# Kernel optimization log

Hardware: AMD Instinct MI355X
Metric: run time of the kernel (lower is better)

Reference implementation:

```python
import jax, jax.numpy as jnp
import numpy as np

DIM = 256
HEADS = 8
HEAD_DIM = DIM // HEADS
EDGE_TYPES = 8  # edge_type_count; table has EDGE_TYPES+1 rows, row 0 is padding
B, N = 2, 2048
EPS = 1e-5


def layer_norm(x, g, b):
    mu = jnp.mean(x, axis=-1, keepdims=True)
    var = jnp.mean(jnp.square(x - mu), axis=-1, keepdims=True)
    return (x - mu) * jax.lax.rsqrt(var + EPS) * g + b


def setup_inputs() -> dict:
    key = jax.random.key(0)
    ks = jax.random.split(key, 12)
    s = 0.02
    x = jax.random.normal(ks[0], (B, N, DIM), dtype=jnp.float32)
    edge_types = jax.random.randint(ks[1], (B, N, N), 0, EDGE_TYPES + 1, dtype=jnp.int32)
    node_mask = jax.random.randint(ks[2], (B, N), 0, 2, dtype=jnp.int32).astype(bool)
    qkv_w = jax.random.normal(ks[3], (DIM, 3 * DIM), dtype=jnp.float32) * s
    qkv_b = jnp.zeros((3 * DIM,), jnp.float32)
    proj_w = jax.random.normal(ks[4], (DIM, DIM), dtype=jnp.float32) * s
    proj_b = jnp.zeros((DIM,), jnp.float32)
    edge_bias_table = jax.random.normal(ks[5], (EDGE_TYPES + 1, HEADS), dtype=jnp.float32) * s
    edge_bias_table = edge_bias_table.at[0].set(0.0)  # padding_idx=0
    ln1_g = jnp.ones((DIM,), jnp.float32); ln1_b = jnp.zeros((DIM,), jnp.float32)
    ln2_g = jnp.ones((DIM,), jnp.float32); ln2_b = jnp.zeros((DIM,), jnp.float32)
    ffn_w1 = jax.random.normal(ks[6], (DIM, 4 * DIM), dtype=jnp.float32) * s
    ffn_b1 = jnp.zeros((4 * DIM,), jnp.float32)
    ffn_w2 = jax.random.normal(ks[7], (4 * DIM, DIM), dtype=jnp.float32) * s
    ffn_b2 = jnp.zeros((DIM,), jnp.float32)
    return dict(x=x, edge_types=edge_types, node_mask=node_mask,
                qkv_w=qkv_w, qkv_b=qkv_b, proj_w=proj_w, proj_b=proj_b,
                edge_bias_table=edge_bias_table, ln1_g=ln1_g, ln1_b=ln1_b,
                ln2_g=ln2_g, ln2_b=ln2_b, ffn_w1=ffn_w1, ffn_b1=ffn_b1,
                ffn_w2=ffn_w2, ffn_b2=ffn_b2)


def reference(x, edge_types, node_mask, qkv_w, qkv_b, proj_w, proj_b,
              edge_bias_table, ln1_g, ln1_b, ln2_g, ln2_b,
              ffn_w1, ffn_b1, ffn_w2, ffn_b2):
    scale = HEAD_DIM ** -0.5
    residual = x
    h = layer_norm(x, ln1_g, ln1_b)
    qkv = h @ qkv_w + qkv_b                         # [B,N,3*DIM]
    qkv = qkv.reshape(B, N, 3, HEADS, HEAD_DIM)
    q, k, v = (qkv[:, :, 0].transpose(0, 2, 1, 3),  # [B,H,N,d]
               qkv[:, :, 1].transpose(0, 2, 1, 3),
               qkv[:, :, 2].transpose(0, 2, 1, 3))
    scores = jnp.einsum('bhnd,bhmd->bhnm', q, k) * scale
    bias = edge_bias_table[edge_types]              # [B,N,N,H]
    scores = scores + bias.transpose(0, 3, 1, 2)    # [B,H,N,N]
    eye = jnp.eye(N, dtype=bool)
    edge_mask = (edge_types != 0) | eye[None]
    node_mask_2d = node_mask[:, None, :] & node_mask[:, :, None]
    attn_mask = edge_mask & node_mask_2d            # [B,N,N]
    scores = jnp.where(attn_mask[:, None], scores, -1e9)
    attn = jax.nn.softmax(scores, axis=-1)
    out = jnp.einsum('bhnm,bhmd->bhnd', attn, v)
    out = out.transpose(0, 2, 1, 3).reshape(B, N, DIM)
    out = (out @ proj_w + proj_b) * node_mask[:, :, None]
    x1 = residual + out
    h2 = layer_norm(x1, ln2_g, ln2_b)
    h2 = jax.nn.gelu(h2 @ ffn_w1 + ffn_b1, approximate=False) @ ffn_w2 + ffn_b2
    h2 = h2 * node_mask[:, :, None]
    return x1 + h2
```

## Files before the change

### kernel.cpp

```cpp
#include <hip/hip_runtime.h>
#include <math.h>

#define DIMM 256
#define HEADS 8
#define NB 2048
#define BB 2
#define ROWS (BB*NB)

typedef __attribute__((ext_vector_type(8))) short bf16x8;
typedef __attribute__((ext_vector_type(4))) short bf16x4;
typedef __attribute__((ext_vector_type(4))) float f32x4;

__device__ inline unsigned short f2bf(float f) {
    unsigned int u = __float_as_uint(f);
    u += 0x7FFFu + ((u >> 16) & 1u);
    return (unsigned short)(u >> 16);
}
__device__ inline float bf2f(unsigned short u) {
    return __uint_as_float(((unsigned int)u) << 16);
}

__device__ inline int get_mask(const void* nm, int fmt, int idx) {
    if (fmt) return ((const unsigned char*)nm)[idx] != 0;
    return ((const int*)nm)[idx] != 0;
}

__device__ inline void ln8_body(const float* __restrict__ x, const float* __restrict__ g,
                                const float* __restrict__ bb, unsigned short* __restrict__ o,
                                int row, int lane32) {
    int c0 = lane32 * 8;
    float4 v0 = *(const float4*)&x[(size_t)row * DIMM + c0];
    float4 v1 = *(const float4*)&x[(size_t)row * DIMM + c0 + 4];
    float s  = v0.x + v0.y + v0.z + v0.w + v1.x + v1.y + v1.z + v1.w;
    float s2 = v0.x*v0.x + v0.y*v0.y + v0.z*v0.z + v0.w*v0.w
             + v1.x*v1.x + v1.y*v1.y + v1.z*v1.z + v1.w*v1.w;
#pragma unroll
    for (int off = 16; off >= 1; off >>= 1) {
        s  += __shfl_xor(s,  off);
        s2 += __shfl_xor(s2, off);
    }
    float mean = s * (1.0f / DIMM);
    float var  = s2 * (1.0f / DIMM) - mean * mean;
    float rstd = rsqrtf(var + 1e-5f);
    float4 g0 = *(const float4*)&g[c0],  g1 = *(const float4*)&g[c0 + 4];
    float4 b0 = *(const float4*)&bb[c0], b1 = *(const float4*)&bb[c0 + 4];
    ushort4 u0, u1;
    u0.x = f2bf((v0.x - mean) * rstd * g0.x + b0.x);
    u0.y = f2bf((v0.y - mean) * rstd * g0.y + b0.y);
    u0.z = f2bf((v0.z - mean) * rstd * g0.z + b0.z);
    u0.w = f2bf((v0.w - mean) * rstd * g0.w + b0.w);
    u1.x = f2bf((v1.x - mean) * rstd * g1.x + b1.x);
    u1.y = f2bf((v1.y - mean) * rstd * g1.y + b1.y);
    u1.z = f2bf((v1.z - mean) * rstd * g1.z + b1.z);
    u1.w = f2bf((v1.w - mean) * rstd * g1.w + b1.w);
    *(ushort4*)&o[(size_t)row * DIMM + c0]     = u0;
    *(ushort4*)&o[(size_t)row * DIMM + c0 + 4] = u1;
}

__global__ __launch_bounds__(256) void prep_kernel(
    const float* __restrict__ w0, const float* __restrict__ w1,
    const float* __restrict__ w2, const float* __restrict__ w3,
    unsigned short* __restrict__ o0, unsigned short* __restrict__ o1,
    unsigned short* __restrict__ o2, unsigned short* __restrict__ o3,
    const float* __restrict__ x, const float* __restrict__ ln1_g,
    const float* __restrict__ ln1_b, unsigned short* __restrict__ h_ln,
    const int* __restrict__ etypes, const void* __restrict__ nmask,
    unsigned char* __restrict__ emaskP)
{
    __shared__ float tile[64][65];
    __shared__ int fsh;
    int bid = blockIdx.x, t = threadIdx.x;
    if (bid < 192) {
        const float* src; unsigned short* dst; int K, N, idx;
        if (bid < 48)       { src = w0; dst = o0; K = 256;  N = 768;  idx = bid; }
        else if (bid < 64)  { src = w1; dst = o1; K = 256;  N = 256;  idx = bid - 48; }
        else if (bid < 128) { src = w2; dst = o2; K = 256;  N = 1024; idx = bid - 64; }
        else                { src = w3; dst = o3; K = 1024; N = 256;  idx = bid - 128; }
        int ntiles = N >> 6;
        int k0 = (idx / ntiles) * 64, n0 = (idx % ntiles) * 64;
        int r = t >> 4, c4 = (t & 15) * 4;
#pragma unroll
        for (int i = 0; i < 4; ++i) {
            float4 v = *(const float4*)&src[(size_t)(k0 + r + i * 16) * N + n0 + c4];
            tile[r + i * 16][c4 + 0] = v.x;
            tile[r + i * 16][c4 + 1] = v.y;
            tile[r + i * 16][c4 + 2] = v.z;
            tile[r + i * 16][c4 + 3] = v.w;
        }
        __syncthreads();
#pragma unroll
        for (int i = 0; i < 4; ++i) {
            int n = n0 + r + i * 16;
            ushort4 u;
            u.x = f2bf(tile[c4 + 0][r + i * 16]);
            u.y = f2bf(tile[c4 + 1][r + i * 16]);
            u.z = f2bf(tile[c4 + 2][r + i * 16]);
            u.w = f2bf(tile[c4 + 3][r + i * 16]);
            *(ushort4*)&dst[(size_t)n * K + k0 + c4] = u;
        }
    } else if (bid < 704) {
        int row = (bid - 192) * 8 + (t >> 5);
        ln8_body(x, ln1_g, ln1_b, h_ln, row, t & 31);
    } else {
        if (t == 0) fsh = 0;
        __syncthreads();
        if (((const unsigned char*)nmask)[4 * t + 1] != 0) fsh = 1;
        __syncthreads();
        int fm = fsh;
        int unit = (bid - 704) * 4 + (t >> 6);
        int lane = t & 63, quad = lane >> 4, l15 = lane & 15;
        int b = unit >> 12;
        int qt16 = (unit >> 5) & 127;
        int kt = unit & 31;
        int qr = qt16 * 16 + l15;
        int rowv = get_mask(nmask, fm, b * NB + qr);
        const int* erow = etypes + (size_t)(b * NB + qr) * NB;
        int dw[4];
#pragma unroll
        for (int t16 = 0; t16 < 4; ++t16) {
            int col0 = kt * 64 + t16 * 16 + quad * 4;
            int4 e4 = *(const int4*)(erow + col0);
            int ee[4] = {e4.x, e4.y, e4.z, e4.w};
            int cv[4];
            if (fm) {
                unsigned int m4 = *(const unsigned int*)((const unsigned char*)nmask + b * NB + col0);
                cv[0] = (m4 & 0xffu) != 0;     cv[1] = (m4 & 0xff00u) != 0;
                cv[2] = (m4 & 0xff0000u) != 0; cv[3] = (m4 >> 24) != 0;
            } else {
                int4 m4 = *(const int4*)((const int*)nmask + b * NB + col0);
                cv[0] = m4.x != 0; cv[1] = m4.y != 0; cv[2] = m4.z != 0; cv[3] = m4.w != 0;
            }
            unsigned int pk = 0u;
#pragma unroll
            for (int r = 0; r < 4; ++r) {
                int col = col0 + r;
                int valid = rowv && cv[r] && ((ee[r] != 0) || (col == qr));
                pk |= (valid ? (unsigned int)(ee[r] + 1) : 0u) << (r * 8);
            }
            dw[t16] = (int)pk;
        }
        int4 o = {dw[0], dw[1], dw[2], dw[3]};
        *(int4*)(emaskP + (size_t)unit * 1024 + lane * 16) = o;
    }
}

__global__ __launch_bounds__(256) void gemm_qkv_mfma(
    const unsigned short* __restrict__ A, const unsigned short* __restrict__ Bt,
    const float* __restrict__ bias,
    unsigned short* __restrict__ qkvh, unsigned short* __restrict__ vT)
{
    const int K = 256;
    int t = threadIdx.x, w = t >> 6, l = t & 63;
    int l15 = l & 15, quad = l >> 4;
    int n0 = blockIdx.x * 64;
    int m0 = blockIdx.y * 64;
    const unsigned short* ap = A + (size_t)(m0 + w * 16 + l15) * K + quad * 8;
    const unsigned short* bp = Bt + (size_t)(n0 + l15) * K + quad * 8;

    f32x4 acc[4];
#pragma unroll
    for (int c = 0; c < 4; ++c) acc[c] = (f32x4){0.f, 0.f, 0.f, 0.f};

    bf16x8 aA, bA[4], aB, bB[4];
    auto ld = [&](bf16x8& af, bf16x8 (&bf)[4], int k0) {
        af = *(const bf16x8*)(ap + k0);
#pragma unroll
        for (int c = 0; c < 4; ++c)
            bf[c] = *(const bf16x8*)(bp + (size_t)(c * 16) * K + k0);
    };
    auto pr = [&](const bf16x8& af, const bf16x8 (&bf)[4]) {
#pragma unroll
        for (int c = 0; c < 4; ++c)
            acc[c] = __builtin_amdgcn_mfma_f32_16x16x32_bf16(af, bf[c], acc[c], 0, 0, 0);
    };
    ld(aA, bA, 0);
    for (int k0 = 0; k0 < K; k0 += 64) {
        ld(aB, bB, k0 + 32);
        pr(aA, bA);
        if (k0 + 64 < K) ld(aA, bA, k0 + 64);
        pr(aB, bB);
    }

    if (n0 < 512) {
        float sc = (n0 < 256) ? 0.17677669529663689f : 1.0f;
#pragma unroll
        for (int r = 0; r < 4; ++r) {
            int row = m0 + w * 16 + quad * 4 + r;
#pragma unroll
            for (int c = 0; c < 4; ++c) {
                int col = n0 + c * 16 + l15;
                qkvh[(size_t)row * 512 + col] = f2bf((acc[c][r] + bias[col]) * sc);
            }
        }
    } else {
        int bb_ = m0 >> 11;
        int n = (m0 + w * 16 + quad * 4) & 2047;
#pragma unroll
        for (int c = 0; c < 4; ++c) {
            int col = n0 + c * 16 + l15 - 512;
            int hidx = col >> 5, d = col & 31;
            float bs = bias[n0 + c * 16 + l15];
            ushort4 u;
            u.x = f2bf(acc[c][0] + bs);
            u.y = f2bf(acc[c][1] + bs);
            u.z = f2bf(acc[c][2] + bs);
            u.w = f2bf(acc[c][3] + bs);
            *(ushort4*)&vT[(size_t)((bb_ * HEADS + hidx) * 32 + d) * NB + n] = u;
        }
    }
}

__global__ __launch_bounds__(256) void attn_mfma(
    const unsigned short* __restrict__ qkvh,
    const unsigned short* __restrict__ vT,
    const unsigned char* __restrict__ emaskP,
    const float* __restrict__ table,
    unsigned short* __restrict__ OpH, float* __restrict__ lpart)
{
    __shared__ unsigned short P[4][16][72];
    __shared__ float tab2m[16];

    int t = threadIdx.x;
    int w = t >> 6, l = t & 63;
    int l15 = l & 15, quad = l >> 4;
    int h = blockIdx.x;
    int qt = blockIdx.y;
    int z = blockIdx.z, b = z >> 2, sp = z & 3;
    int q0 = qt * 64 + w * 16;
    int kbase = sp * (NB / 4);

    if (t < 16) tab2m[t] = (t >= 1 && t < 10) ? __expf(table[(t - 1) * 8 + h]) : 0.f;
    __syncthreads();

    bf16x8 bq = *(const bf16x8*)(qkvh + (size_t)(b * NB + q0 + l15) * 512 + h * 32 + quad * 8);

    const unsigned short* kp = qkvh + (size_t)(b * NB + l15) * 512 + 256 + h * 32 + quad * 8;
    const unsigned short* vp = vT + (size_t)((b * HEADS + h) * 32 + l15) * NB + quad * 8;
    int qt16 = qt * 4 + w;
    const unsigned char* ep = emaskP + (size_t)((b * 128 + qt16) * 32) * 1024 + l * 16;

    float lacc = 0.f;
    f32x4 O0 = {0.f, 0.f, 0.f, 0.f}, O1 = {0.f, 0.f, 0.f, 0.f};

    bf16x8 kA[4], kB[4];
    bf16x8 vA[2][2], vB[2][2];
    int4 eA, eB;

    auto loadtile = [&](bf16x8 (&kf)[4], bf16x8 (&vf)[2][2], int4& ef, int m0) {
#pragma unroll
        for (int t16 = 0; t16 < 4; ++t16)
            kf[t16] = *(const bf16x8*)(kp + (size_t)(m0 + t16 * 16) * 512);
#pragma unroll
        for (int ks = 0; ks < 2; ++ks) {
            vf[ks][0] = *(const bf16x8*)(vp + m0 + ks * 32);
            vf[ks][1] = *(const bf16x8*)(vp + 16 * NB + m0 + ks * 32);
        }
        ef = *(const int4*)(ep + (size_t)(m0 >> 6) * 1024);
    };

    auto process = [&](const bf16x8 (&kf)[4], const bf16x8 (&vf)[2][2], const int4& ef) {
        int ew[4] = {ef.x, ef.y, ef.z, ef.w};
#pragma unroll
        for (int t16 = 0; t16 < 4; ++t16) {
            f32x4 zero = {0.f, 0.f, 0.f, 0.f};
            f32x4 sT = __builtin_amdgcn_mfma_f32_16x16x32_bf16(kf[t16], bq, zero, 0, 0, 0);
            unsigned int e = (unsigned int)ew[t16];
            float p0 = __expf(sT[0]) * tab2m[e & 0xffu];
            float p1 = __expf(sT[1]) * tab2m[(e >> 8) & 0xffu];
            float p2 = __expf(sT[2]) * tab2m[(e >> 16) & 0xffu];
            float p3 = __expf(sT[3]) * tab2m[e >> 24];
            lacc += (p0 + p1) + (p2 + p3);
            bf16x4 pb;
            pb[0] = (short)f2bf(p0); pb[1] = (short)f2bf(p1);
            pb[2] = (short)f2bf(p2); pb[3] = (short)f2bf(p3);
            *(bf16x4*)&P[w][l15][t16 * 16 + quad * 4] = pb;
        }
#pragma unroll
        for (int ks = 0; ks < 2; ++ks) {
            bf16x8 pa = *(const bf16x8*)&P[w][l15][ks * 32 + quad * 8];
            O0 = __builtin_amdgcn_mfma_f32_16x16x32_bf16(pa, vf[ks][0], O0, 0, 0, 0);
            O1 = __builtin_amdgcn_mfma_f32_16x16x32_bf16(pa, vf[ks][1], O1, 0, 0, 0);
        }
    };

    loadtile(kA, vA, eA, kbase);
    for (int m0 = kbase; m0 < kbase + NB / 4; m0 += 128) {
        loadtile(kB, vB, eB, m0 + 64);
        process(kA, vA, eA);
        if (m0 + 128 < kbase + NB / 4) loadtile(kA, vA, eA, m0 + 128);
        process(kB, vB, eB);
    }

    lacc += __shfl_xor(lacc, 16);
    lacc += __shfl_xor(lacc, 32);

    unsigned short* Ob = OpH + (size_t)sp * ROWS * DIMM;
#pragma unroll
    for (int r = 0; r < 4; ++r) {
        int row = b * NB + q0 + quad * 4 + r;
        Ob[(size_t)row * DIMM + h * 32 + l15]      = f2bf(O0[r]);
        Ob[(size_t)row * DIMM + h * 32 + 16 + l15] = f2bf(O1[r]);
    }
    if (quad == 0) {
        int row = b * NB + q0 + l15;
        lpart[(size_t)sp * ROWS * 8 + (size_t)row * 8 + h] = lacc;
    }
}

__global__ __launch_bounds__(1024) void megaback(
    const unsigned short* __restrict__ OpH, const float* __restrict__ lpart,
    const unsigned short* __restrict__ projT, const float* __restrict__ proj_b,
    const float* __restrict__ x, const void* __restrict__ nmask,
    const float* __restrict__ g2, const float* __restrict__ b2,
    const unsigned short* __restrict__ f1T, const float* __restrict__ ffn_b1,
    const unsigned short* __restrict__ f2T, const float* __restrict__ ffn_b2,
    float* __restrict__ out)
{
    __shared__ float rinv_l[16][8];
    __shared__ float stats[16][2];
    __shared__ float redn[16][16][2];
    __shared__ unsigned short Astage[16][264];
    __shared__ float x1s[16][260];
    __shared__ unsigned short hstage[16][264];
    __shared__ unsigned short midstage[16][1032];
    __shared__ int fsh;

    int t = threadIdx.x;
    int w = t >> 6, l = t & 63;
    int l15 = l & 15, quad = l >> 4;
    int grow0 = blockIdx.x * 16;

    if (t == 0) fsh = 0;
    __syncthreads();
    if (((const unsigned char*)nmask)[4 * t + 1] != 0) fsh = 1;

    if (t < 128) {
        int row = t >> 3, h = t & 7;
        float s = 0.f;
#pragma unroll
        for (int sp = 0; sp < 4; ++sp)
            s += lpart[(size_t)sp * ROWS * 8 + (size_t)(grow0 + row) * 8 + h];
        rinv_l[row][h] = (s > 0.f) ? 1.f / s : 0.f;
    }
    __syncthreads();
    int fm = fsh;

    {
        int row = t >> 6, col4 = (t & 63) * 4;
        float rinv = rinv_l[row][col4 >> 5];
        float o0 = 0.f, o1 = 0.f, o2 = 0.f, o3 = 0.f;
#pragma unroll
        for (int sp = 0; sp < 4; ++sp) {
            ushort4 u = *(const ushort4*)&OpH[(size_t)sp * ROWS * DIMM +
                                             (size_t)(grow0 + row) * DIMM + col4];
            o0 += bf2f(u.x); o1 += bf2f(u.y); o2 += bf2f(u.z); o3 += bf2f(u.w);
        }
        ushort4 u;
        u.x = f2bf(o0 * rinv); u.y = f2bf(o1 * rinv);
        u.z = f2bf(o2 * rinv); u.w = f2bf(o3 * rinv);
        *(ushort4*)&Astage[row][col4] = u;
    }
    __syncthreads();

    {
        int col = w * 16 + l15;
        f32x4 acc = (f32x4){0.f, 0.f, 0.f, 0.f};
        const unsigned short* bp = projT + (size_t)col * 256 + quad * 8;
        bf16x8 sb[4];
#pragma unroll
        for (int i = 0; i < 4; ++i) sb[i] = *(const bf16x8*)(bp + i * 32);
#pragma unroll
        for (int ch = 0; ch < 8; ++ch) {
            bf16x8 a = *(const bf16x8*)&Astage[l15][ch * 32 + quad * 8];
            acc = __builtin_amdgcn_mfma_f32_16x16x32_bf16(a, sb[ch & 3], acc, 0, 0, 0);
            if (ch + 4 < 8) sb[ch & 3] = *(const bf16x8*)(bp + (ch + 4) * 32);
        }
        float bs = proj_b[col];
#pragma unroll
        for (int r = 0; r < 4; ++r) {
            int row = quad * 4 + r, grow = grow0 + row;
            float mk = (float)get_mask(nmask, fm, grow);
            float v = (acc[r] + bs) * mk + x[(size_t)grow * DIMM + col];
            x1s[row][col] = v;
            float s = v, s2 = v * v;
#pragma unroll
            for (int off = 1; off < 16; off <<= 1) {
                s += __shfl_xor(s, off); s2 += __shfl_xor(s2, off);
            }
            if (l15 == 0) { redn[row][w][0] = s; redn[row][w][1] = s2; }
        }
    }
    __syncthreads();
    if (t < 16) {
        float s = 0.f, s2 = 0.f;
#pragma unroll
        for (int ww = 0; ww < 16; ++ww) { s += redn[t][ww][0]; s2 += redn[t][ww][1]; }
        float mean = s * (1.f / DIMM);
        float var  = s2 * (1.f / DIMM) - mean * mean;
        stats[t][0] = mean; stats[t][1] = rsqrtf(var + 1e-5f);
    }
    __syncthreads();

    {
        int col = w * 16 + l15;
        float gv = g2[col], bv = b2[col];
#pragma unroll
        for (int r = 0; r < 4; ++r) {
            int row = quad * 4 + r;
            float hv = (x1s[row][col] - stats[row][0]) * stats[row][1] * gv + bv;
            hstage[row][col] = f2bf(hv);
        }
    }
    __syncthreads();

    {
        f32x4 acc[4];
#pragma unroll
        for (int c = 0; c < 4; ++c) acc[c] = (f32x4){0.f, 0.f, 0.f, 0.f};
        const unsigned short* bp = f1T + (size_t)(w * 64 + l15) * 256 + quad * 8;
        bf16x8 bA[4], bB[4];
#pragma unroll
        for (int c = 0; c < 4; ++c) bA[c] = *(const bf16x8*)(bp + (size_t)(c * 16) * 256);
#pragma unroll
        for (int ch = 0; ch < 8; ++ch) {
            bf16x8 a = *(const bf16x8*)&hstage[l15][ch * 32 + quad * 8];
            if (ch + 1 < 8) {
#pragma unroll
                for (int c = 0; c < 4; ++c)
                    bB[c] = *(const bf16x8*)(bp + (size_t)(c * 16) * 256 + (ch + 1) * 32);
            }
#pragma unroll
            for (int c = 0; c < 4; ++c)
                acc[c] = __builtin_amdgcn_mfma_f32_16x16x32_bf16(a, bA[c], acc[c], 0, 0, 0);
#pragma unroll
            for (int c = 0; c < 4; ++c) bA[c] = bB[c];
        }
#pragma unroll
        for (int c = 0; c < 4; ++c) {
            int col = w * 64 + c * 16 + l15;
            float bs = ffn_b1[col];
#pragma unroll
            for (int r = 0; r < 4; ++r) {
                float v = acc[c][r] + bs;
                float x2 = v * v;
                float p = v * fmaf(0.07135481f, x2, 1.5957691f);
                float e = __expf(p);
                float gl = v * (e / (e + 1.f));
                midstage[quad * 4 + r][col] = f2bf(gl);
            }
        }
    }
    __syncthreads();

    {
        int col = w * 16 + l15;
        f32x4 acc = (f32x4){0.f, 0.f, 0.f, 0.f};
        const unsigned short* bp = f2T + (size_t)col * 1024 + quad * 8;
        bf16x8 sb[4];
#pragma unroll
        for (int i = 0; i < 4; ++i) sb[i] = *(const bf16x8*)(bp + i * 32);
#pragma unroll
        for (int ch = 0; ch < 32; ++ch) {
            bf16x8 a = *(const bf16x8*)&midstage[l15][ch * 32 + quad * 8];
            acc = __builtin_amdgcn_mfma_f32_16x16x32_bf16(a, sb[ch & 3], acc, 0, 0, 0);
            if (ch + 4 < 32) sb[ch & 3] = *(const bf16x8*)(bp + (ch + 4) * 32);
        }
        float bs = ffn_b2[col];
#pragma unroll
        for (int r = 0; r < 4; ++r) {
            int row = quad * 4 + r, grow = grow0 + row;
            float mk = (float)get_mask(nmask, fm, grow);
            out[(size_t)grow * DIMM + col] = x1s[row][col] + (acc[r] + bs) * mk;
        }
    }
}

extern "C" void kernel_launch(void* const* d_in, const int* in_sizes, int n_in,
                              void* d_out, int out_size, void* d_ws, size_t ws_size,
                              hipStream_t stream) {
    const float* x       = (const float*)d_in[0];
    const int*   etypes  = (const int*)d_in[1];
    const void*  nmask   = d_in[2];
    const float* qkv_w   = (const float*)d_in[3];
    const float* qkv_b   = (const float*)d_in[4];
    const float* proj_w  = (const float*)d_in[5];
    const float* proj_b  = (const float*)d_in[6];
    const float* table   = (const float*)d_in[7];
    const float* ln1_g   = (const float*)d_in[8];
    const float* ln1_b   = (const float*)d_in[9];
    const float* ln2_g   = (const float*)d_in[10];
    const float* ln2_b   = (const float*)d_in[11];
    const float* ffn_w1  = (const float*)d_in[12];
    const float* ffn_b1  = (const float*)d_in[13];
    const float* ffn_w2  = (const float*)d_in[14];
    const float* ffn_b2  = (const float*)d_in[15];
    float* out = (float*)d_out;
    float* ws  = (float*)d_ws;

    float* lpart = ws;
    unsigned short* ub = (unsigned short*)(ws + 131072);
    unsigned short* h_ln   = ub;
    unsigned short* qkvh   = ub + 1048576;
    unsigned short* vT     = ub + 3145728;
    unsigned short* OpH    = ub + 4194304;
    unsigned short* qkvT   = ub + 8388608;
    unsigned short* projT  = ub + 8585216;
    unsigned short* f1T    = ub + 8650752;
    unsigned short* f2T    = ub + 8912896;
    unsigned char* emaskP  = (unsigned char*)(ub + 9175040);

    prep_kernel<<<dim3(2752), dim3(256), 0, stream>>>(
        qkv_w, proj_w, ffn_w1, ffn_w2, qkvT, projT, f1T, f2T,
        x, ln1_g, ln1_b, h_ln, etypes, nmask, emaskP);
    gemm_qkv_mfma<<<dim3(12, 64), dim3(256), 0, stream>>>(h_ln, qkvT, qkv_b, qkvh, vT);
    attn_mfma<<<dim3(HEADS, NB/64, BB*4), dim3(256), 0, stream>>>(
        qkvh, vT, emaskP, table, OpH, lpart);
    megaback<<<dim3(ROWS/16), dim3(1024), 0, stream>>>(
        OpH, lpart, projT, proj_b, x, nmask, ln2_g, ln2_b,
        f1T, ffn_b1, f2T, ffn_b2, out);
}
```

Before: 230.1 us.

## Pack edge mask to 4-bit codes, halve megaback row tile, add occupancy hints

The precomputed edge-type/mask buffer now packs each entry into 4 bits instead of 8, which halves the mask traffic read by the attention kernel. megaback processes 8 rows per block instead of 16, doubling the grid. The MFMA inputs still use 16 rows, so half of each tile's compute is duplicated and masked off. Register double-buffering in the FFN GEMMs is removed and launch_bounds occupancy hints are added, trading latency hiding for lower register pressure and more resident waves.

```diff
diff --git a/kernel.cpp b/kernel.cpp
--- a/kernel.cpp
+++ b/kernel.cpp
@@ -115,7 +115,7 @@
         int qr = qt16 * 16 + l15;
         int rowv = get_mask(nmask, fm, b * NB + qr);
         const int* erow = etypes + (size_t)(b * NB + qr) * NB;
-        int dw[4];
+        unsigned int dw[2] = {0u, 0u};
 #pragma unroll
         for (int t16 = 0; t16 < 4; ++t16) {
             int col0 = kt * 64 + t16 * 16 + quad * 4;
@@ -130,17 +130,16 @@
                 int4 m4 = *(const int4*)((const int*)nmask + b * NB + col0);
                 cv[0] = m4.x != 0; cv[1] = m4.y != 0; cv[2] = m4.z != 0; cv[3] = m4.w != 0;
             }
-            unsigned int pk = 0u;
 #pragma unroll
             for (int r = 0; r < 4; ++r) {
                 int col = col0 + r;
                 int valid = rowv && cv[r] && ((ee[r] != 0) || (col == qr));
-                pk |= (valid ? (unsigned int)(ee[r] + 1) : 0u) << (r * 8);
-            }
-            dw[t16] = (int)pk;
-        }
-        int4 o = {dw[0], dw[1], dw[2], dw[3]};
-        *(int4*)(emaskP + (size_t)unit * 1024 + lane * 16) = o;
+                unsigned int code = valid ? (unsigned int)(ee[r] + 1) : 0u;
+                dw[t16 >> 1] |= code << ((t16 & 1) * 16 + r * 4);
+            }
+        }
+        int2 o = {(int)dw[0], (int)dw[1]};
+        *(int2*)(emaskP + (size_t)unit * 512 + lane * 8) = o;
     }
 }
 
@@ -210,7 +209,7 @@
     }
 }
 
-__global__ __launch_bounds__(256) void attn_mfma(
+__global__ __launch_bounds__(256, 8) void attn_mfma(
     const unsigned short* __restrict__ qkvh,
     const unsigned short* __restrict__ vT,
     const unsigned char* __restrict__ emaskP,
@@ -237,16 +236,16 @@
     const unsigned short* kp = qkvh + (size_t)(b * NB + l15) * 512 + 256 + h * 32 + quad * 8;
     const unsigned short* vp = vT + (size_t)((b * HEADS + h) * 32 + l15) * NB + quad * 8;
     int qt16 = qt * 4 + w;
-    const unsigned char* ep = emaskP + (size_t)((b * 128 + qt16) * 32) * 1024 + l * 16;
+    const unsigned char* ep = emaskP + (size_t)((b * 128 + qt16) * 32) * 512 + l * 8;
 
     float lacc = 0.f;
     f32x4 O0 = {0.f, 0.f, 0.f, 0.f}, O1 = {0.f, 0.f, 0.f, 0.f};
 
     bf16x8 kA[4], kB[4];
     bf16x8 vA[2][2], vB[2][2];
-    int4 eA, eB;
-
-    auto loadtile = [&](bf16x8 (&kf)[4], bf16x8 (&vf)[2][2], int4& ef, int m0) {
+    int2 eA, eB;
+
+    auto loadtile = [&](bf16x8 (&kf)[4], bf16x8 (&vf)[2][2], int2& ef, int m0) {
 #pragma unroll
         for (int t16 = 0; t16 < 4; ++t16)
             kf[t16] = *(const bf16x8*)(kp + (size_t)(m0 + t16 * 16) * 512);
@@ -255,20 +254,19 @@
             vf[ks][0] = *(const bf16x8*)(vp + m0 + ks * 32);
             vf[ks][1] = *(const bf16x8*)(vp + 16 * NB + m0 + ks * 32);
         }
-        ef = *(const int4*)(ep + (size_t)(m0 >> 6) * 1024);
+        ef = *(const int2*)(ep + (size_t)(m0 >> 6) * 512);
     };
 
-    auto process = [&](const bf16x8 (&kf)[4], const bf16x8 (&vf)[2][2], const int4& ef) {
-        int ew[4] = {ef.x, ef.y, ef.z, ef.w};
+    auto process = [&](const bf16x8 (&kf)[4], const bf16x8 (&vf)[2][2], const int2& ef) {
 #pragma unroll
         for (int t16 = 0; t16 < 4; ++t16) {
             f32x4 zero = {0.f, 0.f, 0.f, 0.f};
             f32x4 sT = __builtin_amdgcn_mfma_f32_16x16x32_bf16(kf[t16], bq, zero, 0, 0, 0);
-            unsigned int e = (unsigned int)ew[t16];
-            float p0 = __expf(sT[0]) * tab2m[e & 0xffu];
-            float p1 = __expf(sT[1]) * tab2m[(e >> 8) & 0xffu];
-            float p2 = __expf(sT[2]) * tab2m[(e >> 16) & 0xffu];
-            float p3 = __expf(sT[3]) * tab2m[e >> 24];
+            unsigned int e = ((unsigned int)((t16 < 2) ? ef.x : ef.y)) >> ((t16 & 1) * 16);
+            float p0 = __expf(sT[0]) * tab2m[e & 0xFu];
+            float p1 = __expf(sT[1]) * tab2m[(e >> 4) & 0xFu];
+            float p2 = __expf(sT[2]) * tab2m[(e >> 8) & 0xFu];
+            float p3 = __expf(sT[3]) * tab2m[(e >> 12) & 0xFu];
             lacc += (p0 + p1) + (p2 + p3);
             bf16x4 pb;
             pb[0] = (short)f2bf(p0); pb[1] = (short)f2bf(p1);
@@ -307,7 +305,7 @@
     }
 }
 
-__global__ __launch_bounds__(1024) void megaback(
+__global__ __launch_bounds__(1024, 8) void megaback(
     const unsigned short* __restrict__ OpH, const float* __restrict__ lpart,
     const unsigned short* __restrict__ projT, const float* __restrict__ proj_b,
     const float* __restrict__ x, const void* __restrict__ nmask,
@@ -316,25 +314,25 @@
     const unsigned short* __restrict__ f2T, const float* __restrict__ ffn_b2,
     float* __restrict__ out)
 {
-    __shared__ float rinv_l[16][8];
-    __shared__ float stats[16][2];
-    __shared__ float redn[16][16][2];
-    __shared__ unsigned short Astage[16][264];
-    __shared__ float x1s[16][260];
-    __shared__ unsigned short hstage[16][264];
-    __shared__ unsigned short midstage[16][1032];
+    __shared__ float rinv_l[8][8];
+    __shared__ float stats[8][2];
+    __shared__ float redn[8][16][2];
+    __shared__ unsigned short Astage[8][264];
+    __shared__ float x1s[8][260];
+    __shared__ unsigned short hstage[8][264];
+    __shared__ unsigned short midstage[8][1032];
     __shared__ int fsh;
 
     int t = threadIdx.x;
     int w = t >> 6, l = t & 63;
     int l15 = l & 15, quad = l >> 4;
-    int grow0 = blockIdx.x * 16;
+    int grow0 = blockIdx.x * 8;
 
     if (t == 0) fsh = 0;
     __syncthreads();
     if (((const unsigned char*)nmask)[4 * t + 1] != 0) fsh = 1;
 
-    if (t < 128) {
+    if (t < 64) {
         int row = t >> 3, h = t & 7;
         float s = 0.f;
 #pragma unroll
@@ -345,7 +343,7 @@
     __syncthreads();
     int fm = fsh;
 
-    {
+    if (t < 512) {
         int row = t >> 6, col4 = (t & 63) * 4;
         float rinv = rinv_l[row][col4 >> 5];
         float o0 = 0.f, o1 = 0.f, o2 = 0.f, o3 = 0.f;
@@ -371,27 +369,30 @@
         for (int i = 0; i < 4; ++i) sb[i] = *(const bf16x8*)(bp + i * 32);
 #pragma unroll
         for (int ch = 0; ch < 8; ++ch) {
-            bf16x8 a = *(const bf16x8*)&Astage[l15][ch * 32 + quad * 8];
+            bf16x8 a = *(const bf16x8*)&Astage[l15 & 7][ch * 32 + quad * 8];
             acc = __builtin_amdgcn_mfma_f32_16x16x32_bf16(a, sb[ch & 3], acc, 0, 0, 0);
             if (ch + 4 < 8) sb[ch & 3] = *(const bf16x8*)(bp + (ch + 4) * 32);
         }
         float bs = proj_b[col];
 #pragma unroll
         for (int r = 0; r < 4; ++r) {
-            int row = quad * 4 + r, grow = grow0 + row;
-            float mk = (float)get_mask(nmask, fm, grow);
-            float v = (acc[r] + bs) * mk + x[(size_t)grow * DIMM + col];
-            x1s[row][col] = v;
-            float s = v, s2 = v * v;
-#pragma unroll
-            for (int off = 1; off < 16; off <<= 1) {
-                s += __shfl_xor(s, off); s2 += __shfl_xor(s2, off);
-            }
-            if (l15 == 0) { redn[row][w][0] = s; redn[row][w][1] = s2; }
-        }
-    }
-    __syncthreads();
-    if (t < 16) {
+            int row16 = quad * 4 + r;
+            if (row16 < 8) {
+                int grow = grow0 + row16;
+                float mk = (float)get_mask(nmask, fm, grow);
+                float v = (acc[r] + bs) * mk + x[(size_t)grow * DIMM + col];
+                x1s[row16][col] = v;
+                float s = v, s2 = v * v;
+#pragma unroll
+                for (int off = 1; off < 16; off <<= 1) {
+                    s += __shfl_xor(s, off); s2 += __shfl_xor(s2, off);
+                }
+                if (l15 == 0) { redn[row16][w][0] = s; redn[row16][w][1] = s2; }
+            }
+        }
+    }
+    __syncthreads();
+    if (t < 8) {
         float s = 0.f, s2 = 0.f;
 #pragma unroll
         for (int ww = 0; ww < 16; ++ww) { s += redn[t][ww][0]; s2 += redn[t][ww][1]; }
@@ -406,9 +407,11 @@
         float gv = g2[col], bv = b2[col];
 #pragma unroll
         for (int r = 0; r < 4; ++r) {
-            int row = quad * 4 + r;
-            float hv = (x1s[row][col] - stats[row][0]) * stats[row][1] * gv + bv;
-            hstage[row][col] = f2bf(hv);
+            int row16 = quad * 4 + r;
+            if (row16 < 8) {
+                float hv = (x1s[row16][col] - stats[row16][0]) * stats[row16][1] * gv + bv;
+                hstage[row16][col] = f2bf(hv);
+            }
         }
     }
     __syncthreads();
@@ -418,22 +421,14 @@
 #pragma unroll
         for (int c = 0; c < 4; ++c) acc[c] = (f32x4){0.f, 0.f, 0.f, 0.f};
         const unsigned short* bp = f1T + (size_t)(w * 64 + l15) * 256 + quad * 8;
-        bf16x8 bA[4], bB[4];
-#pragma unroll
-        for (int c = 0; c < 4; ++c) bA[c] = *(const bf16x8*)(bp + (size_t)(c * 16) * 256);
 #pragma unroll
         for (int ch = 0; ch < 8; ++ch) {
-            bf16x8 a = *(const bf16x8*)&hstage[l15][ch * 32 + quad * 8];
-            if (ch + 1 < 8) {
-#pragma unroll
-                for (int c = 0; c < 4; ++c)
-                    bB[c] = *(const bf16x8*)(bp + (size_t)(c * 16) * 256 + (ch + 1) * 32);
-            }
-#pragma unroll
-            for (int c = 0; c < 4; ++c)
-                acc[c] = __builtin_amdgcn_mfma_f32_16x16x32_bf16(a, bA[c], acc[c], 0, 0, 0);
-#pragma unroll
-            for (int c = 0; c < 4; ++c) bA[c] = bB[c];
+            bf16x8 a = *(const bf16x8*)&hstage[l15 & 7][ch * 32 + quad * 8];
+#pragma unroll
+            for (int c = 0; c < 4; ++c) {
+                bf16x8 bw = *(const bf16x8*)(bp + (size_t)(c * 16) * 256 + ch * 32);
+                acc[c] = __builtin_amdgcn_mfma_f32_16x16x32_bf16(a, bw, acc[c], 0, 0, 0);
+            }
         }
 #pragma unroll
         for (int c = 0; c < 4; ++c) {
@@ -441,12 +436,15 @@
             float bs = ffn_b1[col];
 #pragma unroll
             for (int r = 0; r < 4; ++r) {
-                float v = acc[c][r] + bs;
-                float x2 = v * v;
-                float p = v * fmaf(0.07135481f, x2, 1.5957691f);
-                float e = __expf(p);
-                float gl = v * (e / (e + 1.f));
-                midstage[quad * 4 + r][col] = f2bf(gl);
+                int row16 = quad * 4 + r;
+                if (row16 < 8) {
+                    float v = acc[c][r] + bs;
+                    float x2 = v * v;
+                    float p = v * fmaf(0.07135481f, x2, 1.5957691f);
+                    float e = __expf(p);
+                    float gl = v * (e / (e + 1.f));
+                    midstage[row16][col] = f2bf(gl);
+                }
             }
         }
     }
@@ -454,23 +452,28 @@
 
     {
         int col = w * 16 + l15;
-        f32x4 acc = (f32x4){0.f, 0.f, 0.f, 0.f};
+        f32x4 acc0 = (f32x4){0.f, 0.f, 0.f, 0.f};
+        f32x4 acc1 = (f32x4){0.f, 0.f, 0.f, 0.f};
         const unsigned short* bp = f2T + (size_t)col * 1024 + quad * 8;
-        bf16x8 sb[4];
-#pragma unroll
-        for (int i = 0; i < 4; ++i) sb[i] = *(const bf16x8*)(bp + i * 32);
-#pragma unroll
-        for (int ch = 0; ch < 32; ++ch) {
-            bf16x8 a = *(const bf16x8*)&midstage[l15][ch * 32 + quad * 8];
-            acc = __builtin_amdgcn_mfma_f32_16x16x32_bf16(a, sb[ch & 3], acc, 0, 0, 0);
-            if (ch + 4 < 32) sb[ch & 3] = *(const bf16x8*)(bp + (ch + 4) * 32);
-        }
+#pragma unroll
+        for (int ch = 0; ch < 16; ++ch) {
+            bf16x8 a0 = *(const bf16x8*)&midstage[l15 & 7][ch * 32 + quad * 8];
+            bf16x8 w0 = *(const bf16x8*)(bp + ch * 32);
+            acc0 = __builtin_amdgcn_mfma_f32_16x16x32_bf16(a0, w0, acc0, 0, 0, 0);
+            bf16x8 a1 = *(const bf16x8*)&midstage[l15 & 7][(ch + 16) * 32 + quad * 8];
+            bf16x8 w1 = *(const bf16x8*)(bp + (ch + 16) * 32);
+            acc1 = __builtin_amdgcn_mfma_f32_16x16x32_bf16(a1, w1, acc1, 0, 0, 0);
+        }
+        f32x4 acc = acc0 + acc1;
         float bs = ffn_b2[col];
 #pragma unroll
         for (int r = 0; r < 4; ++r) {
-            int row = quad * 4 + r, grow = grow0 + row;
-            float mk = (float)get_mask(nmask, fm, grow);
-            out[(size_t)grow * DIMM + col] = x1s[row][col] + (acc[r] + bs) * mk;
+            int row16 = quad * 4 + r;
+            if (row16 < 8) {
+                int grow = grow0 + row16;
+                float mk = (float)get_mask(nmask, fm, grow);
+                out[(size_t)grow * DIMM + col] = x1s[row16][col] + (acc[r] + bs) * mk;
+            }
         }
     }
 }
@@ -515,7 +518,7 @@
     gemm_qkv_mfma<<<dim3(12, 64), dim3(256), 0, stream>>>(h_ln, qkvT, qkv_b, qkvh, vT);
     attn_mfma<<<dim3(HEADS, NB/64, BB*4), dim3(256), 0, stream>>>(
         qkvh, vT, emaskP, table, OpH, lpart);
-    megaback<<<dim3(ROWS/16), dim3(1024), 0, stream>>>(
+    megaback<<<dim3(ROWS/8), dim3(1024), 0, stream>>>(
         OpH, lpart, projT, proj_b, x, nmask, ln2_g, ln2_b,
         f1T, ffn_b1, f2T, ffn_b2, out);
 }
```

Result: slower. 364.7 us (+58.5%).

## Compact valid query rows and pack edge codes to 4 bits in attention

Applied to the files above, without the earlier changes.

Adds a scan kernel that counts masked-in nodes per batch, builds a compacted list of valid query row indices, and zeroes lpart for masked-out rows. The edge-mask prep and the attention kernel then iterate only over compacted query tiles and exit early past the valid count. This skips roughly half the query work when about half the nodes are masked. Edge codes are also packed as 4-bit nibbles instead of bytes, halving emaskP traffic. The cost is an extra small serial launch and gather indirection, and rows left unwritten must be handled correctly downstream.

```diff
diff --git a/kernel.cpp b/kernel.cpp
--- a/kernel.cpp
+++ b/kernel.cpp
@@ -23,6 +23,57 @@
 __device__ inline int get_mask(const void* nm, int fmt, int idx) {
     if (fmt) return ((const unsigned char*)nm)[idx] != 0;
     return ((const int*)nm)[idx] != 0;
+}
+
+__global__ __launch_bounds__(256) void scan_kernel(
+    const void* __restrict__ nmask, int* __restrict__ nv,
+    unsigned short* __restrict__ qidx, float* __restrict__ lpart)
+{
+    __shared__ int fsh;
+    __shared__ int cnt[256];
+    __shared__ int base[256];
+    int b = blockIdx.x, t = threadIdx.x;
+    if (t == 0) fsh = 0;
+    __syncthreads();
+    if (((const unsigned char*)nmask)[4 * t + 1] != 0) fsh = 1;
+    __syncthreads();
+    int fm = fsh;
+    int m[8]; int c = 0;
+#pragma unroll
+    for (int i = 0; i < 8; ++i) {
+        m[i] = get_mask(nmask, fm, b * NB + t * 8 + i);
+        c += m[i];
+    }
+    cnt[t] = c;
+    __syncthreads();
+    if (t == 0) {
+        int acc = 0;
+        for (int i = 0; i < 256; ++i) { base[i] = acc; acc += cnt[i]; }
+        nv[b] = acc;
+    }
+    __syncthreads();
+    int off = base[t];
+#pragma unroll
+    for (int i = 0; i < 8; ++i) {
+        int row = t * 8 + i;
+        if (m[i]) {
+            qidx[b * NB + off++] = (unsigned short)row;
+        } else {
+#pragma unroll
+            for (int sp = 0; sp < 4; ++sp) {
+                float* lp = lpart + (size_t)sp * ROWS * 8 + (size_t)(b * NB + row) * 8;
+                *(float4*)lp       = make_float4(0.f, 0.f, 0.f, 0.f);
+                *(float4*)(lp + 4) = make_float4(0.f, 0.f, 0.f, 0.f);
+            }
+        }
+    }
+    __syncthreads();
+    if (t == 0) {
+        int n = nv[b];
+        unsigned short last = (n > 0) ? qidx[b * NB + n - 1] : (unsigned short)0;
+        int padend = (n + 15) & ~15;
+        for (int i = n; i < padend; ++i) qidx[b * NB + i] = last;
+    }
 }
 
 __device__ inline void ln8_body(const float* __restrict__ x, const float* __restrict__ g,
@@ -65,7 +116,8 @@
     const float* __restrict__ x, const float* __restrict__ ln1_g,
     const float* __restrict__ ln1_b, unsigned short* __restrict__ h_ln,
     const int* __restrict__ etypes, const void* __restrict__ nmask,
-    unsigned char* __restrict__ emaskP)
+    unsigned char* __restrict__ emaskP,
+    const int* __restrict__ nv, const unsigned short* __restrict__ qidx)
 {
     __shared__ float tile[64][65];
     __shared__ int fsh;
@@ -112,10 +164,13 @@
         int b = unit >> 12;
         int qt16 = (unit >> 5) & 127;
         int kt = unit & 31;
-        int qr = qt16 * 16 + l15;
-        int rowv = get_mask(nmask, fm, b * NB + qr);
+        int nvb = nv[b];
+        if (qt16 * 16 >= nvb) return;
+        int slot = qt16 * 16 + l15;
+        int validq = slot < nvb;
+        int qr = qidx[b * NB + slot];
         const int* erow = etypes + (size_t)(b * NB + qr) * NB;
-        int dw[4];
+        unsigned int dw[2] = {0u, 0u};
 #pragma unroll
         for (int t16 = 0; t16 < 4; ++t16) {
             int col0 = kt * 64 + t16 * 16 + quad * 4;
@@ -130,17 +185,16 @@
                 int4 m4 = *(const int4*)((const int*)nmask + b * NB + col0);
                 cv[0] = m4.x != 0; cv[1] = m4.y != 0; cv[2] = m4.z != 0; cv[3] = m4.w != 0;
             }
-            unsigned int pk = 0u;
 #pragma unroll
             for (int r = 0; r < 4; ++r) {
                 int col = col0 + r;
-                int valid = rowv && cv[r] && ((ee[r] != 0) || (col == qr));
-                pk |= (valid ? (unsigned int)(ee[r] + 1) : 0u) << (r * 8);
-            }
-            dw[t16] = (int)pk;
-        }
-        int4 o = {dw[0], dw[1], dw[2], dw[3]};
-        *(int4*)(emaskP + (size_t)unit * 1024 + lane * 16) = o;
+                int valid = validq && cv[r] && ((ee[r] != 0) || (col == qr));
+                unsigned int code = valid ? (unsigned int)(ee[r] + 1) : 0u;
+                dw[t16 >> 1] |= code << ((t16 & 1) * 16 + r * 4);
+            }
+        }
+        int2 o = {(int)dw[0], (int)dw[1]};
+        *(int2*)(emaskP + (size_t)unit * 512 + lane * 8) = o;
     }
 }
 
@@ -215,6 +269,7 @@
     const unsigned short* __restrict__ vT,
     const unsigned char* __restrict__ emaskP,
     const float* __restrict__ table,
+    const int* __restrict__ nv, const unsigned short* __restrict__ qidx,
     unsigned short* __restrict__ OpH, float* __restrict__ lpart)
 {
     __shared__ unsigned short P[4][16][72];
@@ -226,27 +281,31 @@
     int h = blockIdx.x;
     int qt = blockIdx.y;
     int z = blockIdx.z, b = z >> 2, sp = z & 3;
-    int q0 = qt * 64 + w * 16;
     int kbase = sp * (NB / 4);
 
     if (t < 16) tab2m[t] = (t >= 1 && t < 10) ? __expf(table[(t - 1) * 8 + h]) : 0.f;
     __syncthreads();
 
-    bf16x8 bq = *(const bf16x8*)(qkvh + (size_t)(b * NB + q0 + l15) * 512 + h * 32 + quad * 8);
+    int nvb = nv[b];
+    int qt16 = qt * 4 + w;
+    int q0c = qt16 * 16;
+    if (q0c >= nvb) return;
+
+    int qrow = b * NB + qidx[b * NB + q0c + l15];
+    bf16x8 bq = *(const bf16x8*)(qkvh + (size_t)qrow * 512 + h * 32 + quad * 8);
 
     const unsigned short* kp = qkvh + (size_t)(b * NB + l15) * 512 + 256 + h * 32 + quad * 8;
     const unsigned short* vp = vT + (size_t)((b * HEADS + h) * 32 + l15) * NB + quad * 8;
-    int qt16 = qt * 4 + w;
-    const unsigned char* ep = emaskP + (size_t)((b * 128 + qt16) * 32) * 1024 + l * 16;
+    const unsigned char* ep = emaskP + (size_t)((b * 128 + qt16) * 32) * 512 + l * 8;
 
     float lacc = 0.f;
     f32x4 O0 = {0.f, 0.f, 0.f, 0.f}, O1 = {0.f, 0.f, 0.f, 0.f};
 
     bf16x8 kA[4], kB[4];
     bf16x8 vA[2][2], vB[2][2];
-    int4 eA, eB;
-
-    auto loadtile = [&](bf16x8 (&kf)[4], bf16x8 (&vf)[2][2], int4& ef, int m0) {
+    int2 eA, eB;
+
+    auto loadtile = [&](bf16x8 (&kf)[4], bf16x8 (&vf)[2][2], int2& ef, int m0) {
 #pragma unroll
         for (int t16 = 0; t16 < 4; ++t16)
             kf[t16] = *(const bf16x8*)(kp + (size_t)(m0 + t16 * 16) * 512);
@@ -255,20 +314,19 @@
             vf[ks][0] = *(const bf16x8*)(vp + m0 + ks * 32);
             vf[ks][1] = *(const bf16x8*)(vp + 16 * NB + m0 + ks * 32);
         }
-        ef = *(const int4*)(ep + (size_t)(m0 >> 6) * 1024);
+        ef = *(const int2*)(ep + (size_t)(m0 >> 6) * 512);
     };
 
-    auto process = [&](const bf16x8 (&kf)[4], const bf16x8 (&vf)[2][2], const int4& ef) {
-        int ew[4] = {ef.x, ef.y, ef.z, ef.w};
+    auto process = [&](const bf16x8 (&kf)[4], const bf16x8 (&vf)[2][2], const int2& ef) {
 #pragma unroll
         for (int t16 = 0; t16 < 4; ++t16) {
             f32x4 zero = {0.f, 0.f, 0.f, 0.f};
             f32x4 sT = __builtin_amdgcn_mfma_f32_16x16x32_bf16(kf[t16], bq, zero, 0, 0, 0);
-            unsigned int e = (unsigned int)ew[t16];
-            float p0 = __expf(sT[0]) * tab2m[e & 0xffu];
-            float p1 = __expf(sT[1]) * tab2m[(e >> 8) & 0xffu];
-            float p2 = __expf(sT[2]) * tab2m[(e >> 16) & 0xffu];
-            float p3 = __expf(sT[3]) * tab2m[e >> 24];
+            unsigned int e = ((unsigned int)((t16 < 2) ? ef.x : ef.y)) >> ((t16 & 1) * 16);
+            float p0 = __expf(sT[0]) * tab2m[e & 0xFu];
+            float p1 = __expf(sT[1]) * tab2m[(e >> 4) & 0xFu];
+            float p2 = __expf(sT[2]) * tab2m[(e >> 8) & 0xFu];
+            float p3 = __expf(sT[3]) * tab2m[(e >> 12) & 0xFu];
             lacc += (p0 + p1) + (p2 + p3);
             bf16x4 pb;
             pb[0] = (short)f2bf(p0); pb[1] = (short)f2bf(p1);
@@ -297,12 +355,15 @@
     unsigned short* Ob = OpH + (size_t)sp * ROWS * DIMM;
 #pragma unroll
     for (int r = 0; r < 4; ++r) {
-        int row = b * NB + q0 + quad * 4 + r;
-        Ob[(size_t)row * DIMM + h * 32 + l15]      = f2bf(O0[r]);
-        Ob[(size_t)row * DIMM + h * 32 + 16 + l15] = f2bf(O1[r]);
-    }
-    if (quad == 0) {
-        int row = b * NB + q0 + l15;
+        int slot = q0c + quad * 4 + r;
+        if (slot < nvb) {
+            int row = b * NB + qidx[b * NB + slot];
+            Ob[(size_t)row * DIMM + h * 32 + l15]      = f2bf(O0[r]);
+            Ob[(size_t)row * DIMM + h * 32 + 16 + l15] = f2bf(O1[r]);
+        }
+    }
+    if (quad == 0 && q0c + l15 < nvb) {
+        int row = b * NB + qidx[b * NB + q0c + l15];
         lpart[(size_t)sp * ROWS * 8 + (size_t)row * 8 + h] = lacc;
     }
 }
@@ -508,13 +569,16 @@
     unsigned short* f1T    = ub + 8650752;
     unsigned short* f2T    = ub + 8912896;
     unsigned char* emaskP  = (unsigned char*)(ub + 9175040);
-
+    unsigned short* qidx   = ub + 11272192;
+    int* nv                = (int*)(ub + 11276288);
+
+    scan_kernel<<<dim3(BB), dim3(256), 0, stream>>>(nmask, nv, qidx, lpart);
     prep_kernel<<<dim3(2752), dim3(256), 0, stream>>>(
         qkv_w, proj_w, ffn_w1, ffn_w2, qkvT, projT, f1T, f2T,
-        x, ln1_g, ln1_b, h_ln, etypes, nmask, emaskP);
+        x, ln1_g, ln1_b, h_ln, etypes, nmask, emaskP, nv, qidx);
     gemm_qkv_mfma<<<dim3(12, 64), dim3(256), 0, stream>>>(h_ln, qkvT, qkv_b, qkvh, vT);
     attn_mfma<<<dim3(HEADS, NB/64, BB*4), dim3(256), 0, stream>>>(
-        qkvh, vT, emaskP, table, OpH, lpart);
+        qkvh, vT, emaskP, table, nv, qidx, OpH, lpart);
     megaback<<<dim3(ROWS/16), dim3(1024), 0, stream>>>(
         OpH, lpart, projT, proj_b, x, nmask, ln2_g, ln2_b,
         f1T, ffn_b1, f2T, ffn_b2, out);
```

Measured after the change: 219.7 us. 1.05x faster.
